# Optimization experiments

Hardware: AMD Instinct MI355X
Metric: run time of the kernel (lower is better)

## Reference

```python
import jax, jax.numpy as jnp
import numpy as np

NP, P, NS = 5, 5, 15  # body parts, joints per part, segments per scale


def _gauss_forward(x):
    # x: (batch, nb_frames, joints=NP*P, coordinates, 1)
    b, T, J, C, _ = x.shape
    inp = x.reshape(b, T, NP, P, C, 1)
    # lengths of the 6 temporal windows: full, two halves, three thirds
    seg_lens = [T, T // 2, T - T // 2, T // 3, T // 3, T - 2 * (T // 3)]
    outs = []
    for L in seg_lens:
        nb_fr = L // NS
        # first NS-1 segments of nb_fr frames each, always starting at frame 0
        head = inp[:, :(NS - 1) * nb_fr].reshape(b, NS - 1, nb_fr, NP, P, C, 1)
        mu_h = head.mean(axis=2)                    # (b, NS-1, NP, P, C, 1)
        xc = head - mu_h[:, :, None]
        cov_h = jnp.einsum('bkfnpci,bkfnpdi->bknpcd', xc, xc) / nb_fr
        # last segment runs to the END of the full sequence (faithful to original)
        tail = inp[:, (NS - 1) * nb_fr:]
        rest = tail.shape[1]
        mu_t = tail.mean(axis=1)                    # (b, NP, P, C, 1)
        xt = tail - mu_t[:, None]
        cov_t = jnp.einsum('bfnpci,bfnpdi->bnpcd', xt, xt) / rest
        mu = jnp.concatenate([mu_h, mu_t[:, None]], axis=1)    # (b, NS, NP, P, C, 1)
        cov = jnp.concatenate([cov_h, cov_t[:, None]], axis=1)  # (b, NS, NP, P, C, C)
        # match torch layout (b, NP, NS, P, ...)
        mu = jnp.transpose(mu, (0, 2, 1, 3, 4, 5))
        cov = jnp.transpose(cov, (0, 2, 1, 3, 4, 5))
        muT = jnp.swapaxes(mu, -1, -2)
        elt00 = cov + mu @ muT                       # E[xx^T]
        ones = jnp.ones(mu.shape[:-2] + (1, 1), dtype=x.dtype)
        top = jnp.concatenate([elt00, mu], axis=-1)
        bot = jnp.concatenate([muT, ones], axis=-1)
        outs.append(jnp.concatenate([top, bot], axis=-2))
    # (b, 6, NP, NS, P, C+1, C+1)
    return jnp.stack(outs, axis=1)


def setup_inputs() -> dict:
    key = jax.random.key(0)
    x = jax.random.normal(key, (256, 2048, 25, 3, 1), dtype=jnp.float32)
    return {"x": x}


def reference(x):
    return _gauss_forward(x)
```

## Files before the change

### kernel.cpp

```cpp
#include <hip/hip_runtime.h>
#include <hip/hip_bf16.h>


__global__ __launch_bounds__(256) void gauss_kernel(const float* __restrict__ x,
                                                    float* __restrict__ out) {
    __shared__ float lds[2250];
    __shared__ float red[225];
    __shared__ float outm[400];

    int bid   = blockIdx.x;
    int chunk = bid % 15;
    int tmp   = bid / 15;
    int stype = tmp % 3;
    int b     = tmp / 3;

    const int nbs[3] = {136, 68, 45};
    int ns = nbs[stype];
    int f0 = chunk * ns;
    int f1 = (chunk == 14) ? 2048 : (f0 + ns);
    float inv_n = 1.0f / (float)(f1 - f0);

    int tid = threadIdx.x;
    if (tid < 250) {
        int j    = tid % 25;
        int tsub = tid / 25;
        const float* base = x + (size_t)b * (2048 * 75) + j * 3;
        float s0=0.f,s1=0.f,s2=0.f,s3=0.f,s4=0.f,s5=0.f,s6=0.f,s7=0.f,s8=0.f;
        for (int t = f0 + tsub; t < f1; t += 10) {
            const float* p = base + t * 75;
            float x0 = p[0], x1 = p[1], x2 = p[2];
            s0 += x0;     s1 += x1;     s2 += x2;
            s3 += x0*x0;  s4 += x0*x1;  s5 += x0*x2;
            s6 += x1*x1;  s7 += x1*x2;  s8 += x2*x2;
        }
        float* l = &lds[tid * 9];
        l[0]=s0; l[1]=s1; l[2]=s2; l[3]=s3; l[4]=s4; l[5]=s5; l[6]=s6; l[7]=s7; l[8]=s8;
    }
    __syncthreads();

    if (tid < 225) {
        int j = tid / 9, si = tid % 9;
        float v = 0.f;
        #pragma unroll
        for (int ts = 0; ts < 10; ++ts) v += lds[(ts * 25 + j) * 9 + si];
        red[j * 9 + si] = v;
    }
    __syncthreads();

    if (tid < 25) {
        const float* r = &red[tid * 9];
        float mu0 = r[0]*inv_n, mu1 = r[1]*inv_n, mu2 = r[2]*inv_n;
        float m00 = r[3]*inv_n, m01 = r[4]*inv_n, m02 = r[5]*inv_n;
        float m11 = r[6]*inv_n, m12 = r[7]*inv_n, m22 = r[8]*inv_n;
        float* o = &outm[tid * 16];
        o[0]=m00; o[1]=m01; o[2]=m02; o[3]=mu0;
        o[4]=m01; o[5]=m11; o[6]=m12; o[7]=mu1;
        o[8]=m02; o[9]=m12; o[10]=m22; o[11]=mu2;
        o[12]=mu0; o[13]=mu1; o[14]=mu2; o[15]=1.0f;
    }
    __syncthreads();

    int so0  = (stype == 0) ? 0 : (stype == 1) ? 1 : 3;
    int ndup = (stype == 0) ? 1 : (stype == 1) ? 2 : 3;
    int total = 400 * ndup;
    size_t obase = (size_t)b * 36000 + (size_t)chunk * 80;
    for (int idx = tid; idx < total; idx += 256) {
        int dup = idx / 400;
        int r   = idx % 400;
        int np  = r / 80;
        int rem = r % 80;
        out[obase + (size_t)(so0 + dup) * 6000 + (size_t)np * 1200 + rem] = outm[r];
    }
}

extern "C" void kernel_launch(void* const* d_in, const int* in_sizes, int n_in,
                              void* d_out, int out_size, void* d_ws, size_t ws_size,
                              hipStream_t stream) {
    const float* x = (const float*)d_in[0];
    float* out = (float*)d_out;
    int blocks = 256 * 3 * 15;
    gauss_kernel<<<blocks, 256, 0, stream>>>(x, out);
}
```

Before: 277.9 us.

## Fuse all window scales into one block per batch with double-buffered LDS streaming

Replaces the per-(batch, scale, chunk) kernel with one 1024-thread block per batch. Each block streams the sequence once through double-buffered LDS using global_load_lds, splitting the frames into pieces at the union of all segment boundaries. Per-piece moment sums are accumulated into ping-pong reduction slots for each scale, and a segment is emitted as float4 rows when its boundary is reached. This removes the re-reading of x for each of the three scales, at the cost of only 256 blocks, many block-wide barriers and serialized piece processing.

```diff
diff --git a/kernel.cpp b/kernel.cpp
--- a/kernel.cpp
+++ b/kernel.cpp
@@ -1,75 +1,166 @@
 #include <hip/hip_runtime.h>
 #include <hip/hip_bf16.h>
+#include <stdint.h>
 
 
-__global__ __launch_bounds__(256) void gauss_kernel(const float* __restrict__ x,
-                                                    float* __restrict__ out) {
-    __shared__ float lds[2250];
-    __shared__ float red[225];
-    __shared__ float outm[400];
+#define NPIECE_MAX 64
+#define IDXPK 0x9210287517640543ull
 
-    int bid   = blockIdx.x;
-    int chunk = bid % 15;
-    int tmp   = bid / 15;
-    int stype = tmp % 3;
-    int b     = tmp / 3;
+struct Tab {
+    int n;
+    uint32_t p[NPIECE_MAX];
+    uint32_t meta[NPIECE_MAX];
+};
 
-    const int nbs[3] = {136, 68, 45};
-    int ns = nbs[stype];
-    int f0 = chunk * ns;
-    int f1 = (chunk == 14) ? 2048 : (f0 + ns);
-    float inv_n = 1.0f / (float)(f1 - f0);
+__global__ __launch_bounds__(1024) void fused_kernel(const float* __restrict__ x,
+                                                     float* __restrict__ out, Tab tab) {
+    __shared__ float sx[2][3760];
+    __shared__ float red[6 * 225 + 16];
+    int tid = threadIdx.x;
+    int b   = blockIdx.x;
+    const float* xb = x + (size_t)b * 153600;
+    int wv = tid >> 6, ln = tid & 63;
 
-    int tid = threadIdx.x;
-    if (tid < 250) {
-        int j    = tid % 25;
-        int tsub = tid / 25;
-        const float* base = x + (size_t)b * (2048 * 75) + j * 3;
-        float s0=0.f,s1=0.f,s2=0.f,s3=0.f,s4=0.f,s5=0.f,s6=0.f,s7=0.f,s8=0.f;
-        for (int t = f0 + tsub; t < f1; t += 10) {
-            const float* p = base + t * 75;
-            float x0 = p[0], x1 = p[1], x2 = p[2];
-            s0 += x0;     s1 += x1;     s2 += x2;
-            s3 += x0*x0;  s4 += x0*x1;  s5 += x0*x2;
-            s6 += x1*x1;  s7 += x1*x2;  s8 += x2*x2;
-        }
-        float* l = &lds[tid * 9];
-        l[0]=s0; l[1]=s1; l[2]=s2; l[3]=s3; l[4]=s4; l[5]=s5; l[6]=s6; l[7]=s7; l[8]=s8;
+    for (int i = tid; i < 6 * 225 + 16; i += 1024) red[i] = 0.f;
+
+    {
+        uint32_t pk = tab.p[0];
+        int f0 = pk & 0xffff, L = (int)(pk >> 16);
+        int w0 = f0 * 75, base_f = w0 & ~3;
+        int nv4 = (w0 - base_f + L * 75 + 3) >> 2;
+        const float4* src = (const float4*)(xb + base_f);
+        int i = wv * 64 + ln;
+        if (i < nv4)
+            __builtin_amdgcn_global_load_lds(
+                (const __attribute__((address_space(1))) void*)(src + i),
+                (__attribute__((address_space(3))) void*)(&sx[0][wv * 256]), 16, 0, 0);
     }
+
+    int cell = tid >> 2, q = tid & 3;
+    int j  = cell / 9, si = cell - j * 9;
+    int k3 = si - 3;
+    int ia = (si < 3) ? si : (k3 < 3 ? 0 : (k3 < 5 ? 1 : 2));
+    int ib = (si < 3) ? si : (k3 < 3 ? k3 : (k3 < 5 ? k3 - 2 : 2));
+    bool single = (si < 3);
+    int off0 = q * 75 + j * 3;
+
     __syncthreads();
 
-    if (tid < 225) {
-        int j = tid / 9, si = tid % 9;
-        float v = 0.f;
-        #pragma unroll
-        for (int ts = 0; ts < 10; ++ts) v += lds[(ts * 25 + j) * 9 + si];
-        red[j * 9 + si] = v;
+    int n = tab.n;
+    for (int p = 0; p < n; ++p) {
+        uint32_t pk = tab.p[p];
+        int f0 = pk & 0xffff, L = (int)(pk >> 16);
+        int shift = (f0 * 75) & 3;
+        int buf = p & 1;
+
+        if (p + 1 < n) {
+            uint32_t pk2 = tab.p[p + 1];
+            int g0 = pk2 & 0xffff, L2 = (int)(pk2 >> 16);
+            int w0 = g0 * 75, base_f = w0 & ~3;
+            int nv4 = (w0 - base_f + L2 * 75 + 3) >> 2;
+            const float4* src = (const float4*)(xb + base_f);
+            int i = wv * 64 + ln;
+            if (i < nv4)
+                __builtin_amdgcn_global_load_lds(
+                    (const __attribute__((address_space(1))) void*)(src + i),
+                    (__attribute__((address_space(3))) void*)(&sx[buf ^ 1][wv * 256]), 16, 0, 0);
+        }
+
+        uint32_t mt = tab.meta[p];
+        if (tid < 900) {
+            const float* s = &sx[buf][shift];
+            float acc = 0.f;
+            int off = off0;
+            for (int t = q; t < L; t += 4, off += 300) {
+                float a  = s[off + ia];
+                float bb = s[off + ib];
+                acc += single ? a : a * bb;
+            }
+            acc += __shfl_xor(acc, 1);
+            acc += __shfl_xor(acc, 2);
+            if (q == 0) {
+                int c0 = mt & 15, c1 = (mt >> 4) & 15, c2 = (mt >> 8) & 15;
+                red[((c0 & 1)) * 225 + cell]     += acc;
+                red[(2 + (c1 & 1)) * 225 + cell] += acc;
+                red[(4 + (c2 & 1)) * 225 + cell] += acc;
+            }
+        }
+
+        uint32_t em = (mt >> 12) & 7;
+        if (em) {
+            __syncthreads();
+            float4* ob4 = (float4*)(out + (size_t)b * 36000);
+            for (int st = 0; st < 3; ++st) {
+                if (!((em >> st) & 1)) continue;
+                int ch  = (mt >> (4 * st)) & 15;
+                int ns  = (st == 0) ? 136 : (st == 1) ? 68 : 45;
+                int nfr = (ch == 14) ? (2048 - 14 * ns) : ns;
+                float inv = 1.0f / (float)nfr;
+                int slot = st * 2 + (ch & 1);
+                int ndup = st + 1;
+                int so0  = (st == 0) ? 0 : (st == 1) ? 1 : 3;
+                int tot  = ndup * 100;
+                for (int i2 = tid; i2 < tot; i2 += 1024) {
+                    int dup = i2 / 100;
+                    int r2  = i2 - dup * 100;
+                    int jj  = r2 >> 2, r = r2 & 3;
+                    int np_ = jj / 5, pp = jj - np_ * 5;
+                    const float* rb = &red[slot * 225 + jj * 9];
+                    uint64_t pkk = IDXPK >> (16 * r);
+                    float4 v;
+                    v.x = rb[(int)(pkk & 15)] * inv;
+                    v.y = rb[(int)((pkk >> 4) & 15)] * inv;
+                    v.z = rb[(int)((pkk >> 8) & 15)] * inv;
+                    v.w = (r == 3) ? 1.0f : rb[(int)((pkk >> 12) & 15)] * inv;
+                    ob4[(so0 + dup) * 1500 + np_ * 300 + ch * 20 + pp * 4 + r] = v;
+                }
+            }
+            __syncthreads();
+            if (tid < 225) {
+                for (int st = 0; st < 3; ++st) {
+                    if (!((em >> st) & 1)) continue;
+                    int ch = (mt >> (4 * st)) & 15;
+                    red[(st * 2 + (ch & 1)) * 225 + tid] = 0.f;
+                }
+            }
+        }
+        __syncthreads();
     }
-    __syncthreads();
+}
 
-    if (tid < 25) {
-        const float* r = &red[tid * 9];
-        float mu0 = r[0]*inv_n, mu1 = r[1]*inv_n, mu2 = r[2]*inv_n;
-        float m00 = r[3]*inv_n, m01 = r[4]*inv_n, m02 = r[5]*inv_n;
-        float m11 = r[6]*inv_n, m12 = r[7]*inv_n, m22 = r[8]*inv_n;
-        float* o = &outm[tid * 16];
-        o[0]=m00; o[1]=m01; o[2]=m02; o[3]=mu0;
-        o[4]=m01; o[5]=m11; o[6]=m12; o[7]=mu1;
-        o[8]=m02; o[9]=m12; o[10]=m22; o[11]=mu2;
-        o[12]=mu0; o[13]=mu1; o[14]=mu2; o[15]=1.0f;
+static void build_tab(Tab& tab) {
+    unsigned char isb[2049];
+    for (int i = 0; i <= 2048; ++i) isb[i] = 0;
+    isb[2048] = 1;
+    for (int k = 1; k <= 14; ++k) { isb[45 * k] = 1; isb[68 * k] = 1; isb[136 * k] = 1; }
+    int n = 0, prev = 0;
+    for (int f = 1; f <= 2048; ++f) {
+        if (!isb[f]) continue;
+        int len = f - prev;
+        int npc = (len + 49) / 50;
+        int base = len / npc, rem = len % npc;
+        int s = prev;
+        for (int i = 0; i < npc && n < NPIECE_MAX; ++i) {
+            int l = base + (i < rem ? 1 : 0);
+            tab.p[n++] = (uint32_t)(s | (l << 16));
+            s += l;
+        }
+        prev = f;
     }
-    __syncthreads();
-
-    int so0  = (stype == 0) ? 0 : (stype == 1) ? 1 : 3;
-    int ndup = (stype == 0) ? 1 : (stype == 1) ? 2 : 3;
-    int total = 400 * ndup;
-    size_t obase = (size_t)b * 36000 + (size_t)chunk * 80;
-    for (int idx = tid; idx < total; idx += 256) {
-        int dup = idx / 400;
-        int r   = idx % 400;
-        int np  = r / 80;
-        int rem = r % 80;
-        out[obase + (size_t)(so0 + dup) * 6000 + (size_t)np * 1200 + rem] = outm[r];
+    tab.n = n;
+    const int nst[3] = {136, 68, 45};
+    for (int i = 0; i < n; ++i) {
+        int f0 = tab.p[i] & 0xffff;
+        int f1 = f0 + (int)(tab.p[i] >> 16);
+        uint32_t m = 0;
+        for (int st = 0; st < 3; ++st) {
+            int ns = nst[st];
+            int c = f0 / ns; if (c > 14) c = 14;
+            int bnd = (c == 14) ? 2048 : (c + 1) * ns;
+            m |= (uint32_t)c << (4 * st);
+            if (f1 == bnd) m |= 1u << (12 + st);
+        }
+        tab.meta[i] = m;
     }
 }
 
@@ -78,6 +169,7 @@
                               hipStream_t stream) {
     const float* x = (const float*)d_in[0];
     float* out = (float*)d_out;
-    int blocks = 256 * 3 * 15;
-    gauss_kernel<<<blocks, 256, 0, stream>>>(x, out);
+    Tab tab;
+    build_tab(tab);
+    fused_kernel<<<256, 1024, 0, stream>>>(x, out, tab);
 }
```

Measured after the change: 251.0 us. 1.11x faster.
